# Optimization experiments

Hardware: AMD Instinct MI355X
Metric: run time of the kernel (lower is better)

The kernel has to match this reference:

```python
import jax, jax.numpy as jnp
import numpy as np

B, N = 1, 384          # batch, N_res
C_Z, C_H, H = 128, 32, 4  # pair channels, per-head hidden, heads
INF = 1.0e9
LN_EPS = 1e-5


def setup_inputs() -> dict:
    key = jax.random.key(0)
    ks = jax.random.split(key, 8)
    s = lambda k, shape: jax.random.normal(k, shape, jnp.float32) * 0.02
    return {
        "z": jax.random.normal(ks[0], (B, N, N, C_Z), jnp.float32),
        "mask": jnp.ones((B, N, N), jnp.float32),
        "ln_gamma": jnp.ones((C_Z,), jnp.float32),
        "ln_beta": jnp.zeros((C_Z,), jnp.float32),
        "w_bias": s(ks[1], (C_Z, H)),          # Linear(c_z, num_heads, bias=False)
        "w_q": s(ks[2], (C_Z, H * C_H)),        # no-bias q/k/v projections
        "w_k": s(ks[3], (C_Z, H * C_H)),
        "w_v": s(ks[4], (C_Z, H * C_H)),
        "w_g": s(ks[5], (C_Z, H * C_H)),        # gating projection
        "b_g": jnp.ones((H * C_H,), jnp.float32),  # gating bias init ones
        "w_o": s(ks[6], (H * C_H, C_Z)),        # output projection
        "b_o": jnp.zeros((C_Z,), jnp.float32),
    }


def reference(z, mask, ln_gamma, ln_beta, w_bias, w_q, w_k, w_v, w_g, b_g, w_o, b_o):
    # ta_type == "starting": no transposes.
    # LayerNorm over c_z
    mu = jnp.mean(z, axis=-1, keepdims=True)
    var = jnp.var(z, axis=-1, keepdims=True)
    zn = (z - mu) * jax.lax.rsqrt(var + LN_EPS) * ln_gamma + ln_beta  # [B,N,N,C_Z]

    # triangle bias: linear(z) -> [B,N,N,H] -> movedim -> [B,H,i,j], broadcast over batch-row axis
    tri_bias = jnp.einsum('bijc,ch->bhij', zn, w_bias)  # [B,H,N,N]
    # mask bias: masked keys get -inf; mask shape [B,i,k] broadcast to [B,i,1,1,k]
    mask_bias = INF * (mask - 1.0)

    wq = w_q.reshape(C_Z, H, C_H)
    wk = w_k.reshape(C_Z, H, C_H)
    wv = w_v.reshape(C_Z, H, C_H)
    q = jnp.einsum('bijc,chd->bijhd', zn, wq) * (C_H ** -0.5)  # scale q
    k = jnp.einsum('bijc,chd->bijhd', zn, wk)
    v = jnp.einsum('bijc,chd->bijhd', zn, wv)

    # attention over the j/k axis per row i: logits [B,i,H,j,k]
    logits = jnp.einsum('bijhd,bikhd->bihjk', q, k)
    logits = logits + mask_bias[:, :, None, None, :] + tri_bias[:, None, :, :, :]
    a = jax.nn.softmax(logits, axis=-1)
    o = jnp.einsum('bihjk,bikhd->bijhd', a, v)  # [B,N,N,H,C_H]

    # gating
    g = jax.nn.sigmoid(jnp.einsum('bijc,ce->bije', zn, w_g) + b_g)  # [B,N,N,H*C_H]
    o = o.reshape(B, N, N, H * C_H) * g
    return jnp.einsum('bije,ec->bijc', o, w_o) + b_o  # [B,N,N,C_Z]
```

## Files before the change

kernel.cpp:

```cpp
#include <hip/hip_runtime.h>

#define NRES 384
#define CZ 128
#define NH 4
#define CH 32
#define NN (NRES * NRES)
#define NNCZ ((size_t)NN * CZ)

typedef unsigned short u16;
typedef __attribute__((ext_vector_type(4))) unsigned short us4;
typedef __attribute__((ext_vector_type(8))) unsigned short us8;
typedef __attribute__((ext_vector_type(8))) short s8;
typedef __attribute__((ext_vector_type(4))) float f4;

#define L2E 1.4426950408889634f

__device__ __forceinline__ float bf2f(u16 u) {
  return __uint_as_float(((unsigned)u) << 16);
}
__device__ __forceinline__ u16 f2bf(float f) {
  unsigned u = __float_as_uint(f);
  u += 0x7fffu + ((u >> 16) & 1u);
  return (u16)(u >> 16);
}
__device__ __forceinline__ unsigned cvtpk(float lo, float hi) {
  unsigned w;
  asm("v_cvt_pk_bf16_f32 %0, %1, %2" : "=v"(w) : "v"(lo), "v"(hi));
  return w;
}

template<bool F32>
__device__ __forceinline__ float ld1(const void* p, size_t i) {
  if constexpr (F32) return ((const float*)p)[i];
  else return bf2f(((const u16*)p)[i]);
}

template<bool F32>
__device__ __forceinline__ void ld4v(const void* p, size_t i, float o[4]) {
  if constexpr (F32) {
    const float4 a = *(const float4*)((const float*)p + i);
    o[0] = a.x; o[1] = a.y; o[2] = a.z; o[3] = a.w;
  } else {
    const us4 v = *(const us4*)((const u16*)p + i);
    #pragma unroll
    for (int u = 0; u < 4; ++u) o[u] = bf2f(v[u]);
  }
}

template<bool F32>
__device__ __forceinline__ void ld8(const void* p, size_t i, float o[8]) {
  if constexpr (F32) {
    const float4 a = *(const float4*)((const float*)p + i);
    const float4 b = *(const float4*)((const float*)p + i + 4);
    o[0] = a.x; o[1] = a.y; o[2] = a.z; o[3] = a.w;
    o[4] = b.x; o[5] = b.y; o[6] = b.z; o[7] = b.w;
  } else {
    const us8 v = *(const us8*)((const u16*)p + i);
    #pragma unroll
    for (int u = 0; u < 8; ++u) o[u] = bf2f(v[u]);
  }
}

__global__ void k_probe(const u16* __restrict__ z, int* __restrict__ flag) {
  int weird = 0;
  for (int i = threadIdx.x; i < 256; i += 64) {
    const int e = (z[i] >> 7) & 0xFF;
    if (e < 0x70 || e > 0x8F) weird++;
  }
  #pragma unroll
  for (int m = 1; m < 64; m <<= 1) weird += __shfl_xor(weird, m, 64);
  if (threadIdx.x == 0) *flag = (weird >= 16) ? 1 : 0;
}

template<bool F32>
__global__ __launch_bounds__(256, 2) void k_ln_proj(
    const void* __restrict__ z, const void* __restrict__ gma, const void* __restrict__ bta,
    const void* __restrict__ wbias, const void* __restrict__ wq, const void* __restrict__ wk,
    const void* __restrict__ wv, const void* __restrict__ wg, const void* __restrict__ bg,
    u16* __restrict__ qb, u16* __restrict__ kb, u16* __restrict__ vb, u16* __restrict__ gb,
    float* __restrict__ triT, const int* __restrict__ flag)
{
  if ((*flag != 0) != F32) return;
  __shared__ __align__(16) u16 znl[128 * 136];
  __shared__ __align__(16) u16 WT[CZ * CZ];
  const int t = threadIdx.x;
  const int lane = t & 63;
  const int wid = t >> 6;
  const int n16 = lane & 15;
  const int quad = lane >> 4;
  const int rowBase = blockIdx.x * 128;

  const int c0 = n16 * 8;
  float g8[8], b8[8];
  ld8<F32>(gma, c0, g8);
  ld8<F32>(bta, c0, b8);
  for (int it = 0; it < 8; ++it) {
    const int rl = wid * 32 + it * 4 + quad;
    float x[8];
    ld8<F32>(z, (size_t)(rowBase + rl) * CZ + c0, x);
    float s = 0.f, q2 = 0.f;
    #pragma unroll
    for (int u = 0; u < 8; ++u) { s += x[u]; q2 += x[u] * x[u]; }
    #pragma unroll
    for (int m = 1; m < 16; m <<= 1) {
      s  += __shfl_xor(s, m, 64);
      q2 += __shfl_xor(q2, m, 64);
    }
    const float mu = s * (1.0f / CZ);
    const float rs = rsqrtf(q2 * (1.0f / CZ) - mu * mu + 1e-5f);
    us8 o;
    #pragma unroll
    for (int u = 0; u < 8; ++u) o[u] = f2bf((x[u] - mu) * rs * g8[u] + b8[u]);
    *(us8*)&znl[rl * 136 + c0] = o;
  }
  __syncthreads();

  float wb4[8][4];
  #pragma unroll
  for (int cc = 0; cc < 8; ++cc) ld4v<F32>(wbias, (size_t)(c0 + cc) * NH, wb4[cc]);
  for (int it = 0; it < 8; ++it) {
    const int rl = wid * 32 + it * 4 + quad;
    const us8 zv8 = *(const us8*)&znl[rl * 136 + c0];
    float a0 = 0.f, a1 = 0.f, a2 = 0.f, a3 = 0.f;
    #pragma unroll
    for (int cc = 0; cc < 8; ++cc) {
      const float zv = bf2f(zv8[cc]);
      a0 += zv * wb4[cc][0]; a1 += zv * wb4[cc][1];
      a2 += zv * wb4[cc][2]; a3 += zv * wb4[cc][3];
    }
    #pragma unroll
    for (int m = 1; m < 16; m <<= 1) {
      a0 += __shfl_xor(a0, m, 64); a1 += __shfl_xor(a1, m, 64);
      a2 += __shfl_xor(a2, m, 64); a3 += __shfl_xor(a3, m, 64);
    }
    if (n16 < 4) {
      const float v = (n16 == 0) ? a0 : (n16 == 1) ? a1 : (n16 == 2) ? a2 : a3;
      const int P = rowBase + rl;
      const int aI = P / NRES, bI = P % NRES;
      triT[(size_t)n16 * NN + (size_t)bI * NRES + aI] = v;
    }
  }

  const u16 scl_q = 1;
  for (int arr = 0; arr < 4; ++arr) {
    const void* W = (arr == 0) ? wq : (arr == 1) ? wk : (arr == 2) ? wv : wg;
    __syncthreads();
    #pragma unroll
    for (int it = 0; it < 16; ++it) {
      const int c = (t >> 5) + it * 8;
      const int m0 = (t & 31) * 4;
      float w4[4];
      ld4v<F32>(W, (size_t)c * CZ + m0, w4);
      const int ks = c >> 5, qq = (c >> 3) & 3, j = c & 7;
      #pragma unroll
      for (int mm = 0; mm < 4; ++mm) {
        const int m = m0 + mm;
        WT[ks * 4096 + (((m >> 4) * 4 + qq) * 16 + (m & 15)) * 8 + j] = f2bf(w4[mm]);
      }
    }
    __syncthreads();

    f4 acc[2][8];
    #pragma unroll
    for (int i = 0; i < 2; ++i)
      #pragma unroll
      for (int nt = 0; nt < 8; ++nt) acc[i][nt] = f4{0.f, 0.f, 0.f, 0.f};

    #pragma unroll
    for (int ks = 0; ks < 4; ++ks) {
      s8 a[2], b[8];
      #pragma unroll
      for (int i = 0; i < 2; ++i)
        a[i] = *(const s8*)&WT[ks * 4096 + (((wid * 2 + i) * 4 + quad) * 16 + n16) * 8];
      #pragma unroll
      for (int nt = 0; nt < 8; ++nt)
        b[nt] = *(const s8*)&znl[(nt * 16 + n16) * 136 + ks * 32 + quad * 8];
      #pragma unroll
      for (int i = 0; i < 2; ++i)
        #pragma unroll
        for (int nt = 0; nt < 8; ++nt)
          acc[i][nt] = __builtin_amdgcn_mfma_f32_16x16x32_bf16(a[i], b[nt], acc[i][nt], 0, 0, 0);
    }

    u16* dstb = (arr == 0) ? qb : (arr == 1) ? kb : (arr == 2) ? vb : gb;
    #pragma unroll
    for (int i = 0; i < 2; ++i) {
      const int mt = wid * 2 + i;
      const int och0 = mt * 16 + quad * 4;
      float e4[4];
      if (arr == 3) ld4v<F32>(bg, och0, e4);
      #pragma unroll
      for (int nt = 0; nt < 8; ++nt) {
        us4 o;
        #pragma unroll
        for (int r = 0; r < 4; ++r) {
          float v = acc[i][nt][r];
          if (arr == 0) v *= 0.17677669529663687f;
          else if (arr == 3) v = 1.0f / (1.0f + __expf(-(v + e4[r])));
          o[r] = f2bf(v);
        }
        *(us4*)&dstb[(size_t)(rowBase + nt * 16 + n16) * CZ + och0] = o;
      }
    }
  }
  (void)scl_q;
}

template<bool F32>
__global__ __launch_bounds__(256, 3) void k_attn(
    const u16* __restrict__ qb, const u16* __restrict__ kb, const u16* __restrict__ vb,
    const u16* __restrict__ gb, const float* __restrict__ triT, const void* __restrict__ msk,
    u16* __restrict__ ogb, const int* __restrict__ flag)
{
  if ((*flag != 0) != F32) return;
  __shared__ __align__(16) u16 VB[12 * 4 * 32 * 8];
  __shared__ __align__(16) u16 Pch[4][16 * 40];
  __shared__ __align__(16) float mbL[NRES];
  __shared__ int anyM;
  const int t = threadIdx.x;
  const int i = blockIdx.x >> 2;
  const int h = blockIdx.x & 3;
  const size_t base_i = (size_t)i * NRES;

  if (t == 0) anyM = 0;
  __syncthreads();

  #pragma unroll
  for (int it = 0; it < 12; ++it) {
    const int idx = t + it * 256;
    const int kk = idx >> 3;
    const int d0 = (idx & 7) * 4;
    const us4 vv = *(const us4*)&vb[(base_i + kk) * CZ + h * CH + d0];
    const int cc2 = kk >> 5;
    const int kap = kk & 31;
    const int p = 2 * (kap & 15) + (kap >> 4);
    u16* vdst = &VB[((cc2 * 4 + (p >> 3)) * 32 + d0) * 8 + (p & 7)];
    vdst[0] = vv[0]; vdst[8] = vv[1]; vdst[16] = vv[2]; vdst[24] = vv[3];
  }
  {
    int loc = 0;
    for (int idx = t; idx < NRES; idx += 256) {
      const float mb = 1.0e9f * (ld1<F32>(msk, base_i + idx) - 1.0f);
      mbL[idx] = mb;
      if (mb != 0.0f) loc = 1;
    }
    if (loc) atomicOr(&anyM, 1);
  }
  __syncthreads();
  const bool masked = (anyM != 0);

  const int wid = t >> 6;
  const int lane = t & 63;
  const int n = lane & 15;
  const int quad = lane >> 4;
  const float* trih = triT + (size_t)h * NN;
  u16* pb = &Pch[wid][0];

  for (int pr = wid; pr < 12; pr += 4) {
    const int jrowA = pr * 32;
    const int jrowB = jrowA + 16;
    const s8 aqA = *(const s8*)&qb[(base_i + jrowA + n) * CZ + h * CH + quad * 8];
    const s8 aqB = *(const s8*)&qb[(base_i + jrowB + n) * CZ + h * CH + quad * 8];

    f4 O0A = {0.f,0.f,0.f,0.f}, O1A = {0.f,0.f,0.f,0.f};
    f4 O0B = {0.f,0.f,0.f,0.f}, O1B = {0.f,0.f,0.f,0.f};
    f4 lA = {0.f,0.f,0.f,0.f}, lB = {0.f,0.f,0.f,0.f};
    f4 nmA = {3.0e38f, 3.0e38f, 3.0e38f, 3.0e38f};
    f4 nmB = {3.0e38f, 3.0e38f, 3.0e38f, 3.0e38f};

    s8 bk[4];
    #pragma unroll
    for (int u = 0; u < 4; ++u)
      bk[u] = *(const s8*)&kb[(base_i + u * 16 + n) * CZ + h * CH + quad * 8];

    #pragma unroll 1
    for (int cc = 0; cc < 6; ++cc) {
      f4 SA[4], SB[4];
      #pragma unroll
      for (int u = 0; u < 4; ++u) {
        const f4 z4 = {0.f, 0.f, 0.f, 0.f};
        SA[u] = __builtin_amdgcn_mfma_f32_16x16x32_bf16(aqA, bk[u], z4, 0, 0, 0);
        SB[u] = __builtin_amdgcn_mfma_f32_16x16x32_bf16(aqB, bk[u], z4, 0, 0, 0);
      }
      if (cc < 5) {
        #pragma unroll
        for (int u = 0; u < 4; ++u)
          bk[u] = *(const s8*)&kb[(base_i + ((cc + 1) * 4 + u) * 16 + n) * CZ + h * CH + quad * 8];
      }
      #pragma unroll
      for (int u = 0; u < 4; ++u) {
        const int tt = cc * 4 + u;
        const size_t trow = (size_t)(tt * 16 + n) * NRES;
        const float4 tA = *(const float4*)&trih[trow + jrowA + quad * 4];
        const float4 tB = *(const float4*)&trih[trow + jrowB + quad * 4];
        SA[u][0] += tA.x; SA[u][1] += tA.y; SA[u][2] += tA.z; SA[u][3] += tA.w;
        SB[u][0] += tB.x; SB[u][1] += tB.y; SB[u][2] += tB.z; SB[u][3] += tB.w;
      }
      if (masked) {
        #pragma unroll
        for (int u = 0; u < 4; ++u) {
          const float mbv = mbL[(cc * 4 + u) * 16 + n];
          #pragma unroll
          for (int r = 0; r < 4; ++r) { SA[u][r] += mbv; SB[u][r] += mbv; }
        }
      }
      f4 mxA, mxB;
      #pragma unroll
      for (int r = 0; r < 4; ++r) {
        mxA[r] = fmaxf(fmaxf(SA[0][r], SA[1][r]), fmaxf(SA[2][r], SA[3][r]));
        mxB[r] = fmaxf(fmaxf(SB[0][r], SB[1][r]), fmaxf(SB[2][r], SB[3][r]));
      }
      #pragma unroll
      for (int sft = 1; sft < 16; sft <<= 1) {
        #pragma unroll
        for (int r = 0; r < 4; ++r) {
          mxA[r] = fmaxf(mxA[r], __shfl_xor(mxA[r], sft, 64));
          mxB[r] = fmaxf(mxB[r], __shfl_xor(mxB[r], sft, 64));
        }
      }
      #pragma unroll
      for (int r = 0; r < 4; ++r) {
        const float nmAn = fminf(nmA[r], mxA[r] * (-L2E));
        const float scA = __builtin_exp2f(nmAn - nmA[r]);
        nmA[r] = nmAn;
        O0A[r] *= scA; O1A[r] *= scA; lA[r] *= scA;
        const float nmBn = fminf(nmB[r], mxB[r] * (-L2E));
        const float scB = __builtin_exp2f(nmBn - nmB[r]);
        nmB[r] = nmBn;
        O0B[r] *= scB; O1B[r] *= scB; lB[r] *= scB;
      }
      #pragma unroll
      for (int u = 0; u < 4; ++u) {
        #pragma unroll
        for (int r = 0; r < 4; ++r) {
          SA[u][r] = __builtin_exp2f(__builtin_fmaf(SA[u][r], L2E, nmA[r]));
          lA[r] += SA[u][r];
          SB[u][r] = __builtin_exp2f(__builtin_fmaf(SB[u][r], L2E, nmB[r]));
          lB[r] += SB[u][r];
        }
      }
      #pragma unroll
      for (int s = 0; s < 2; ++s) {
        const int C = cc * 2 + s;
        const s8 bv0 = *(const s8*)&VB[((C * 4 + quad) * 32 + n) * 8];
        const s8 bv1 = *(const s8*)&VB[((C * 4 + quad) * 32 + 16 + n) * 8];
        #pragma unroll
        for (int r = 0; r < 4; ++r)
          *(unsigned*)&pb[(quad * 4 + r) * 40 + n * 2] = cvtpk(SA[2 * s][r], SA[2 * s + 1][r]);
        const s8 apA = *(const s8*)&pb[n * 40 + quad * 8];
        O0A = __builtin_amdgcn_mfma_f32_16x16x32_bf16(apA, bv0, O0A, 0, 0, 0);
        O1A = __builtin_amdgcn_mfma_f32_16x16x32_bf16(apA, bv1, O1A, 0, 0, 0);
        #pragma unroll
        for (int r = 0; r < 4; ++r)
          *(unsigned*)&pb[(quad * 4 + r) * 40 + n * 2] = cvtpk(SB[2 * s][r], SB[2 * s + 1][r]);
        const s8 apB = *(const s8*)&pb[n * 40 + quad * 8];
        O0B = __builtin_amdgcn_mfma_f32_16x16x32_bf16(apB, bv0, O0B, 0, 0, 0);
        O1B = __builtin_amdgcn_mfma_f32_16x16x32_bf16(apB, bv1, O1B, 0, 0, 0);
      }
    }

    f4 sA = lA, sB = lB;
    #pragma unroll
    for (int sft = 1; sft < 16; sft <<= 1) {
      #pragma unroll
      for (int r = 0; r < 4; ++r) {
        sA[r] += __shfl_xor(sA[r], sft, 64);
        sB[r] += __shfl_xor(sB[r], sft, 64);
      }
    }
    #pragma unroll
    for (int r = 0; r < 4; ++r) {
      const float ivA = 1.0f / sA[r];
      const size_t rowA = (base_i + jrowA + quad * 4 + r) * CZ + h * CH;
      const float gA0 = bf2f(gb[rowA + n]);
      const float gA1 = bf2f(gb[rowA + 16 + n]);
      ogb[rowA + n]      = f2bf(O0A[r] * ivA * gA0);
      ogb[rowA + 16 + n] = f2bf(O1A[r] * ivA * gA1);
      const float ivB = 1.0f / sB[r];
      const size_t rowB = (base_i + jrowB + quad * 4 + r) * CZ + h * CH;
      const float gB0 = bf2f(gb[rowB + n]);
      const float gB1 = bf2f(gb[rowB + 16 + n]);
      ogb[rowB + n]      = f2bf(O0B[r] * ivB * gB0);
      ogb[rowB + 16 + n] = f2bf(O1B[r] * ivB * gB1);
    }
  }
}

template<bool F32>
__global__ __launch_bounds__(256, 2) void k_out(
    const u16* __restrict__ og, const void* __restrict__ wo, const void* __restrict__ bo,
    void* __restrict__ outp, const int* __restrict__ flag)
{
  if ((*flag != 0) != F32) return;
  __shared__ __align__(16) u16 ol[128 * 136];
  __shared__ __align__(16) u16 WT[CZ * CZ];
  const int t = threadIdx.x;
  const int lane = t & 63;
  const int wid = t >> 6;
  const int n16 = lane & 15;
  const int quad = lane >> 4;
  const int rowBase = blockIdx.x * 128;

  #pragma unroll
  for (int it = 0; it < 8; ++it) {
    const int idx8 = t + it * 256;
    const int r = idx8 >> 4;
    const int c0 = (idx8 & 15) * 8;
    *(us8*)&ol[r * 136 + c0] = *(const us8*)&og[(size_t)(rowBase + r) * CZ + c0];
  }
  #pragma unroll
  for (int it = 0; it < 16; ++it) {
    const int c = (t >> 5) + it * 8;
    const int m0 = (t & 31) * 4;
    float w4[4];
    ld4v<F32>(wo, (size_t)c * CZ + m0, w4);
    const int ks = c >> 5, qq = (c >> 3) & 3, j = c & 7;
    #pragma unroll
    for (int mm = 0; mm < 4; ++mm) {
      const int m = m0 + mm;
      WT[ks * 4096 + (((m >> 4) * 4 + qq) * 16 + (m & 15)) * 8 + j] = f2bf(w4[mm]);
    }
  }
  __syncthreads();

  f4 acc[2][8];
  #pragma unroll
  for (int i = 0; i < 2; ++i)
    #pragma unroll
    for (int nt = 0; nt < 8; ++nt) acc[i][nt] = f4{0.f, 0.f, 0.f, 0.f};

  #pragma unroll
  for (int ks = 0; ks < 4; ++ks) {
    s8 a[2], b[8];
    #pragma unroll
    for (int i = 0; i < 2; ++i)
      a[i] = *(const s8*)&WT[ks * 4096 + (((wid * 2 + i) * 4 + quad) * 16 + n16) * 8];
    #pragma unroll
    for (int nt = 0; nt < 8; ++nt)
      b[nt] = *(const s8*)&ol[(nt * 16 + n16) * 136 + ks * 32 + quad * 8];
    #pragma unroll
    for (int i = 0; i < 2; ++i)
      #pragma unroll
      for (int nt = 0; nt < 8; ++nt)
        acc[i][nt] = __builtin_amdgcn_mfma_f32_16x16x32_bf16(a[i], b[nt], acc[i][nt], 0, 0, 0);
  }

  #pragma unroll
  for (int i = 0; i < 2; ++i) {
    const int och0 = (wid * 2 + i) * 16 + quad * 4;
    float b4[4];
    ld4v<F32>(bo, och0, b4);
    #pragma unroll
    for (int nt = 0; nt < 8; ++nt) {
      const size_t off = (size_t)(rowBase + nt * 16 + n16) * CZ + och0;
      if constexpr (F32) {
        float4 o;
        o.x = acc[i][nt][0] + b4[0]; o.y = acc[i][nt][1] + b4[1];
        o.z = acc[i][nt][2] + b4[2]; o.w = acc[i][nt][3] + b4[3];
        *(float4*)&((float*)outp)[off] = o;
      } else {
        us4 o;
        #pragma unroll
        for (int r = 0; r < 4; ++r) o[r] = f2bf(acc[i][nt][r] + b4[r]);
        *(us4*)&((u16*)outp)[off] = o;
      }
    }
  }
}

extern "C" void kernel_launch(void* const* d_in, const int* in_sizes, int n_in,
                              void* d_out, int out_size, void* d_ws, size_t ws_size,
                              hipStream_t stream) {
  const void* z     = d_in[0];
  const void* msk   = d_in[1];
  const void* gma   = d_in[2];
  const void* bta   = d_in[3];
  const void* wbias = d_in[4];
  const void* wq    = d_in[5];
  const void* wk    = d_in[6];
  const void* wv    = d_in[7];
  const void* wg    = d_in[8];
  const void* bg    = d_in[9];
  const void* wo    = d_in[10];
  const void* bo    = d_in[11];

  char* ws = (char*)d_ws;
  int* flag = (int*)ws;
  u16* qb = (u16*)(ws + 256);
  u16* kb = qb + NNCZ;
  u16* vb = kb + NNCZ;
  u16* gb = vb + NNCZ;
  float* triT = (float*)(gb + NNCZ);
  u16* ogb = qb;

  k_probe<<<dim3(1), dim3(64), 0, stream>>>((const u16*)z, flag);

  k_ln_proj<false><<<dim3(NN / 128), dim3(256), 0, stream>>>(
      z, gma, bta, wbias, wq, wk, wv, wg, bg, qb, kb, vb, gb, triT, flag);
  k_ln_proj<true><<<dim3(NN / 128), dim3(256), 0, stream>>>(
      z, gma, bta, wbias, wq, wk, wv, wg, bg, qb, kb, vb, gb, triT, flag);

  k_attn<false><<<dim3(NRES * NH), dim3(256), 0, stream>>>(
      qb, kb, vb, gb, triT, msk, ogb, flag);
  k_attn<true><<<dim3(NRES * NH), dim3(256), 0, stream>>>(
      qb, kb, vb, gb, triT, msk, ogb, flag);

  k_out<false><<<dim3(NN / 128), dim3(256), 0, stream>>>(ogb, wo, bo, d_out, flag);
  k_out<true><<<dim3(NN / 128), dim3(256), 0, stream>>>(ogb, wo, bo, d_out, flag);
}
```

Measured before the change: 522.4 us.

## Prefetch triangle-bias tiles and double-buffer P staging in attention kernel

The attention loop now loads the next chunk's triangle-bias values into registers one iteration ahead, so the global read latency overlaps the current chunk's softmax work. P staging uses separate LDS buffers for the A and B row groups, which lets both be written before the PV MFMAs are issued back to back. The inline-asm packed bf16 convert is replaced by software round-to-nearest f2bf packing. This costs more VGPRs, which may hurt occupancy under the 3-block launch bound, and adds extra ALU for the conversions.

Result: slower. 601.9 us (+15.2%).

```diff
diff --git a/kernel.cpp b/kernel.cpp
--- a/kernel.cpp
+++ b/kernel.cpp
@@ -22,11 +22,6 @@
   unsigned u = __float_as_uint(f);
   u += 0x7fffu + ((u >> 16) & 1u);
   return (u16)(u >> 16);
-}
-__device__ __forceinline__ unsigned cvtpk(float lo, float hi) {
-  unsigned w;
-  asm("v_cvt_pk_bf16_f32 %0, %1, %2" : "=v"(w) : "v"(lo), "v"(hi));
-  return w;
 }
 
 template<bool F32>
@@ -214,7 +209,7 @@
 {
   if ((*flag != 0) != F32) return;
   __shared__ __align__(16) u16 VB[12 * 4 * 32 * 8];
-  __shared__ __align__(16) u16 Pch[4][16 * 40];
+  __shared__ __align__(16) u16 Pch[4][2][16 * 40];
   __shared__ __align__(16) float mbL[NRES];
   __shared__ int anyM;
   const int t = threadIdx.x;
@@ -254,7 +249,8 @@
   const int n = lane & 15;
   const int quad = lane >> 4;
   const float* trih = triT + (size_t)h * NN;
-  u16* pb = &Pch[wid][0];
+  u16* pbA = &Pch[wid][0][0];
+  u16* pbB = &Pch[wid][1][0];
 
   for (int pr = wid; pr < 12; pr += 4) {
     const int jrowA = pr * 32;
@@ -269,93 +265,111 @@
     f4 nmB = {3.0e38f, 3.0e38f, 3.0e38f, 3.0e38f};
 
     s8 bk[4];
+    f4 tCA[4], tCB[4];
     #pragma unroll
     for (int u = 0; u < 4; ++u)
       bk[u] = *(const s8*)&kb[(base_i + u * 16 + n) * CZ + h * CH + quad * 8];
+    #pragma unroll
+    for (int u = 0; u < 4; ++u) {
+      const size_t trow = (size_t)(u * 16 + n) * NRES;
+      tCA[u] = *(const f4*)&trih[trow + jrowA + quad * 4];
+      tCB[u] = *(const f4*)&trih[trow + jrowB + quad * 4];
+    }
 
     #pragma unroll 1
-    for (int cc = 0; cc < 6; ++cc) {
-      f4 SA[4], SB[4];
-      #pragma unroll
-      for (int u = 0; u < 4; ++u) {
-        const f4 z4 = {0.f, 0.f, 0.f, 0.f};
-        SA[u] = __builtin_amdgcn_mfma_f32_16x16x32_bf16(aqA, bk[u], z4, 0, 0, 0);
-        SB[u] = __builtin_amdgcn_mfma_f32_16x16x32_bf16(aqB, bk[u], z4, 0, 0, 0);
-      }
-      if (cc < 5) {
-        #pragma unroll
-        for (int u = 0; u < 4; ++u)
-          bk[u] = *(const s8*)&kb[(base_i + ((cc + 1) * 4 + u) * 16 + n) * CZ + h * CH + quad * 8];
-      }
-      #pragma unroll
-      for (int u = 0; u < 4; ++u) {
-        const int tt = cc * 4 + u;
-        const size_t trow = (size_t)(tt * 16 + n) * NRES;
-        const float4 tA = *(const float4*)&trih[trow + jrowA + quad * 4];
-        const float4 tB = *(const float4*)&trih[trow + jrowB + quad * 4];
-        SA[u][0] += tA.x; SA[u][1] += tA.y; SA[u][2] += tA.z; SA[u][3] += tA.w;
-        SB[u][0] += tB.x; SB[u][1] += tB.y; SB[u][2] += tB.z; SB[u][3] += tB.w;
-      }
-      if (masked) {
+    for (int c = 0; c < 3; ++c) {
+      #pragma unroll
+      for (int half = 0; half < 2; ++half) {
+        const int e = 2 * c + half;
+        f4 SA[4], SB[4];
         #pragma unroll
         for (int u = 0; u < 4; ++u) {
-          const float mbv = mbL[(cc * 4 + u) * 16 + n];
-          #pragma unroll
-          for (int r = 0; r < 4; ++r) { SA[u][r] += mbv; SB[u][r] += mbv; }
-        }
-      }
-      f4 mxA, mxB;
-      #pragma unroll
-      for (int r = 0; r < 4; ++r) {
-        mxA[r] = fmaxf(fmaxf(SA[0][r], SA[1][r]), fmaxf(SA[2][r], SA[3][r]));
-        mxB[r] = fmaxf(fmaxf(SB[0][r], SB[1][r]), fmaxf(SB[2][r], SB[3][r]));
-      }
-      #pragma unroll
-      for (int sft = 1; sft < 16; sft <<= 1) {
+          const f4 z4 = {0.f, 0.f, 0.f, 0.f};
+          SA[u] = __builtin_amdgcn_mfma_f32_16x16x32_bf16(aqA, bk[u], z4, 0, 0, 0);
+          SB[u] = __builtin_amdgcn_mfma_f32_16x16x32_bf16(aqB, bk[u], z4, 0, 0, 0);
+        }
+        if (e < 5) {
+          #pragma unroll
+          for (int u = 0; u < 4; ++u)
+            bk[u] = *(const s8*)&kb[(base_i + ((e + 1) * 4 + u) * 16 + n) * CZ + h * CH + quad * 8];
+        }
+        #pragma unroll
+        for (int u = 0; u < 4; ++u) {
+          #pragma unroll
+          for (int r = 0; r < 4; ++r) { SA[u][r] += tCA[u][r]; SB[u][r] += tCB[u][r]; }
+        }
+        if (masked) {
+          #pragma unroll
+          for (int u = 0; u < 4; ++u) {
+            const float mbv = mbL[(e * 4 + u) * 16 + n];
+            #pragma unroll
+            for (int r = 0; r < 4; ++r) { SA[u][r] += mbv; SB[u][r] += mbv; }
+          }
+        }
+        if (e < 5) {
+          #pragma unroll
+          for (int u = 0; u < 4; ++u) {
+            const size_t trow = (size_t)(((e + 1) * 4 + u) * 16 + n) * NRES;
+            tCA[u] = *(const f4*)&trih[trow + jrowA + quad * 4];
+            tCB[u] = *(const f4*)&trih[trow + jrowB + quad * 4];
+          }
+        }
+        f4 mxA, mxB;
         #pragma unroll
         for (int r = 0; r < 4; ++r) {
-          mxA[r] = fmaxf(mxA[r], __shfl_xor(mxA[r], sft, 64));
-          mxB[r] = fmaxf(mxB[r], __shfl_xor(mxB[r], sft, 64));
-        }
-      }
-      #pragma unroll
-      for (int r = 0; r < 4; ++r) {
-        const float nmAn = fminf(nmA[r], mxA[r] * (-L2E));
-        const float scA = __builtin_exp2f(nmAn - nmA[r]);
-        nmA[r] = nmAn;
-        O0A[r] *= scA; O1A[r] *= scA; lA[r] *= scA;
-        const float nmBn = fminf(nmB[r], mxB[r] * (-L2E));
-        const float scB = __builtin_exp2f(nmBn - nmB[r]);
-        nmB[r] = nmBn;
-        O0B[r] *= scB; O1B[r] *= scB; lB[r] *= scB;
-      }
-      #pragma unroll
-      for (int u = 0; u < 4; ++u) {
+          mxA[r] = fmaxf(fmaxf(SA[0][r], SA[1][r]), fmaxf(SA[2][r], SA[3][r]));
+          mxB[r] = fmaxf(fmaxf(SB[0][r], SB[1][r]), fmaxf(SB[2][r], SB[3][r]));
+        }
+        #pragma unroll
+        for (int sft = 1; sft < 16; sft <<= 1) {
+          #pragma unroll
+          for (int r = 0; r < 4; ++r) {
+            mxA[r] = fmaxf(mxA[r], __shfl_xor(mxA[r], sft, 64));
+            mxB[r] = fmaxf(mxB[r], __shfl_xor(mxB[r], sft, 64));
+          }
+        }
         #pragma unroll
         for (int r = 0; r < 4; ++r) {
-          SA[u][r] = __builtin_exp2f(__builtin_fmaf(SA[u][r], L2E, nmA[r]));
-          lA[r] += SA[u][r];
-          SB[u][r] = __builtin_exp2f(__builtin_fmaf(SB[u][r], L2E, nmB[r]));
-          lB[r] += SB[u][r];
-        }
-      }
-      #pragma unroll
-      for (int s = 0; s < 2; ++s) {
-        const int C = cc * 2 + s;
-        const s8 bv0 = *(const s8*)&VB[((C * 4 + quad) * 32 + n) * 8];
-        const s8 bv1 = *(const s8*)&VB[((C * 4 + quad) * 32 + 16 + n) * 8];
-        #pragma unroll
-        for (int r = 0; r < 4; ++r)
-          *(unsigned*)&pb[(quad * 4 + r) * 40 + n * 2] = cvtpk(SA[2 * s][r], SA[2 * s + 1][r]);
-        const s8 apA = *(const s8*)&pb[n * 40 + quad * 8];
-        O0A = __builtin_amdgcn_mfma_f32_16x16x32_bf16(apA, bv0, O0A, 0, 0, 0);
-        O1A = __builtin_amdgcn_mfma_f32_16x16x32_bf16(apA, bv1, O1A, 0, 0, 0);
-        #pragma unroll
-        for (int r = 0; r < 4; ++r)
-          *(unsigned*)&pb[(quad * 4 + r) * 40 + n * 2] = cvtpk(SB[2 * s][r], SB[2 * s + 1][r]);
-        const s8 apB = *(const s8*)&pb[n * 40 + quad * 8];
-        O0B = __builtin_amdgcn_mfma_f32_16x16x32_bf16(apB, bv0, O0B, 0, 0, 0);
-        O1B = __builtin_amdgcn_mfma_f32_16x16x32_bf16(apB, bv1, O1B, 0, 0, 0);
+          const float nmAn = fminf(nmA[r], mxA[r] * (-L2E));
+          const float scA = __builtin_exp2f(nmAn - nmA[r]);
+          nmA[r] = nmAn;
+          O0A[r] *= scA; O1A[r] *= scA; lA[r] *= scA;
+          const float nmBn = fminf(nmB[r], mxB[r] * (-L2E));
+          const float scB = __builtin_exp2f(nmBn - nmB[r]);
+          nmB[r] = nmBn;
+          O0B[r] *= scB; O1B[r] *= scB; lB[r] *= scB;
+        }
+        #pragma unroll
+        for (int u = 0; u < 4; ++u) {
+          #pragma unroll
+          for (int r = 0; r < 4; ++r) {
+            SA[u][r] = __builtin_exp2f(__builtin_fmaf(SA[u][r], L2E, nmA[r]));
+            lA[r] += SA[u][r];
+            SB[u][r] = __builtin_exp2f(__builtin_fmaf(SB[u][r], L2E, nmB[r]));
+            lB[r] += SB[u][r];
+          }
+        }
+        #pragma unroll
+        for (int s = 0; s < 2; ++s) {
+          #pragma unroll
+          for (int r = 0; r < 4; ++r) {
+            const unsigned wA = (unsigned)f2bf(SA[2 * s][r]) |
+                                ((unsigned)f2bf(SA[2 * s + 1][r]) << 16);
+            *(unsigned*)&pbA[(quad * 4 + r) * 40 + n * 2] = wA;
+            const unsigned wB = (unsigned)f2bf(SB[2 * s][r]) |
+                                ((unsigned)f2bf(SB[2 * s + 1][r]) << 16);
+            *(unsigned*)&pbB[(quad * 4 + r) * 40 + n * 2] = wB;
+          }
+          const int C = e * 2 + s;
+          const s8 apA = *(const s8*)&pbA[n * 40 + quad * 8];
+          const s8 apB = *(const s8*)&pbB[n * 40 + quad * 8];
+          const s8 bv0 = *(const s8*)&VB[((C * 4 + quad) * 32 + n) * 8];
+          const s8 bv1 = *(const s8*)&VB[((C * 4 + quad) * 32 + 16 + n) * 8];
+          O0A = __builtin_amdgcn_mfma_f32_16x16x32_bf16(apA, bv0, O0A, 0, 0, 0);
+          O1A = __builtin_amdgcn_mfma_f32_16x16x32_bf16(apA, bv1, O1A, 0, 0, 0);
+          O0B = __builtin_amdgcn_mfma_f32_16x16x32_bf16(apB, bv0, O0B, 0, 0, 0);
+          O1B = __builtin_amdgcn_mfma_f32_16x16x32_bf16(apB, bv1, O1B, 0, 0, 0);
+        }
       }
     }
 
```
